# Kernel tuning notes

Hardware: AMD Instinct MI355X
Metric: run time of the kernel (lower is better)

The kernel has to match this reference:

```python
import jax, jax.numpy as jnp
import numpy as np

N = 20000      # n_nodes
L = 4          # lamb_len (number of decay rates)
M = 64         # memory_dimension (= message_dimension)
F = 128        # node feature dim
E = 128        # embedding_dimension
B = 100000     # number of interaction events in the batch
RAW = 2 * M * L + F + 1  # 641, raw message dim
H = RAW // 2   # MLP hidden dim


def setup_inputs() -> dict:
    key = jax.random.key(0)
    ks = jax.random.split(key, 18)
    s = lambda d: 1.0 / np.sqrt(d)
    inp = {
        "node_features": jax.random.normal(ks[0], (N, F), jnp.float32),
        "memory": jax.random.normal(ks[1], (N, L, M), jnp.float32) * 0.1,
        "last_update": jnp.zeros((N,), jnp.float32),
        "lambs": jnp.array([1.0, 0.1, 0.01, 0.001], jnp.float32),
        "theta": jnp.array([0.5], jnp.float32),
        "static_emb": jax.random.normal(ks[2], (N, E), jnp.float32),
        "W1": jax.random.normal(ks[3], (H, RAW), jnp.float32) * s(RAW),
        "b1": jnp.zeros((H,), jnp.float32),
        "W2": jax.random.normal(ks[4], (M, H), jnp.float32) * s(H),
        "b2": jnp.zeros((M,), jnp.float32),
        "We": jax.random.normal(ks[5], (M, L * M), jnp.float32) * s(L * M),
        "be": jnp.zeros((M,), jnp.float32),
        "Ws": jax.random.normal(ks[6], (E, M), jnp.float32) * s(M),
        "bs": jnp.zeros((E,), jnp.float32),
        "timestamps": jax.random.uniform(ks[7], (B,), jnp.float32) * 1000.0,
        "source_nodes": jax.random.randint(ks[8], (B,), 0, N),
        "target_nodes": jax.random.randint(ks[9], (B,), 0, N),
    }
    return inp


def reference(node_features, memory, last_update, lambs, theta, static_emb,
              W1, b1, W2, b2, We, be, Ws, bs,
              timestamps, source_nodes, target_nodes):
    n, l, m = memory.shape
    b = source_nodes.shape[0]
    mem_flat = memory.reshape(n, l * m)

    # ---- temporal memory gather + raw message build: [B, RAW] ----
    src_emb = mem_flat[source_nodes]
    tgt_emb = mem_flat[target_nodes]
    raw = jnp.concatenate(
        [src_emb, tgt_emb, node_features[target_nodes],
         jnp.ones((b, 1), memory.dtype)], axis=1)

    # ---- exp_lambs aggregation per source node ----
    t_node = jax.ops.segment_max(timestamps, source_nodes, num_segments=n)
    counts = jax.ops.segment_sum(jnp.ones_like(timestamps), source_nodes,
                                 num_segments=n)
    has = counts > 0
    t_node_safe = jnp.where(has, t_node, last_update)  # latest event time per node
    dt = t_node_safe[source_nodes] - timestamps        # [B], >= 0
    w = jnp.exp(-dt[:, None] * lambs[None, :])         # [B, L] decay weights
    # decayed sum of raw messages per node, per lambda: [N, L, RAW]
    agg = jnp.stack(
        [jax.ops.segment_sum(w[:, li:li + 1] * raw, source_nodes,
                             num_segments=n) for li in range(l)], axis=1)

    # ---- MLP message function: [N, L, M] ----
    h = jax.nn.relu(jnp.einsum('nlr,hr->nlh', agg, W1) + b1)
    msg = jnp.einsum('nlh,mh->nlm', h, W2) + b2

    # ---- exp memory update ----
    decay = jnp.exp(-(t_node_safe - last_update)[:, None] * lambs[None, :])  # [N, L]
    updated = memory * decay[..., None] + jnp.where(has[:, None, None], msg, 0.0)

    # ---- embedding fusion ----
    dyn = updated.reshape(n, l * m)
    e = jax.nn.leaky_relu(dyn @ We.T + be, negative_slope=0.01)
    s = jax.nn.leaky_relu(e @ Ws.T + bs, negative_slope=0.01)
    embeddings = theta * static_emb + (1.0 - theta) * s
    return embeddings
```

## Files before the change

### kernel.cpp

```cpp
#include <hip/hip_runtime.h>

constexpr int LDIM = 4;
constexpr int MDIM = 64;
constexpr int FDIM = 128;
constexpr int EDIM = 128;
constexpr int RAWD = 641;
constexpr int HDIM = 320;
constexpr int LM   = LDIM * MDIM;
constexpr int KXY  = LM + FDIM;
constexpr int NXY  = 2 * HDIM;

typedef _Float16 f16x8 __attribute__((ext_vector_type(8)));
typedef _Float16 f16x4 __attribute__((ext_vector_type(4)));
typedef float    f32x4 __attribute__((ext_vector_type(4)));

constexpr float WSCALE  = 256.f;
constexpr float WSINV   = 1.f / 256.f;

__global__ void k_init(int* t_node_bits, int* counts, int* cursor2, int* cursor, int Nn)
{
    int n = blockIdx.x * blockDim.x + threadIdx.x;
    if (n < Nn) {
        t_node_bits[n] = 0xBF800000;
        counts[n]  = 0;
        cursor2[n] = 0;
    }
    if (n == 0) cursor[0] = 0;
}

__global__ void k_ev1(const int* __restrict__ src, const float* __restrict__ ts,
                      int* t_node_bits, int* counts, int Bev)
{
    int b = blockIdx.x * blockDim.x + threadIdx.x;
    if (b >= Bev) return;
    int s = src[b];
    atomicMax(&t_node_bits[s], __float_as_int(ts[b]));
    atomicAdd(&counts[s], 1);
}

__global__ void k_node(const int* __restrict__ t_node_bits, const int* __restrict__ counts,
                       const float* __restrict__ last_update, const float* __restrict__ lambs,
                       float* t_safe, float* decay, int* start, int* cursor, int Nn)
{
    int n = blockIdx.x * blockDim.x + threadIdx.x;
    if (n >= Nn) return;
    int c = counts[n];
    float lu = last_update[n];
    float tsn = (c > 0) ? __int_as_float(t_node_bits[n]) : lu;
    t_safe[n] = tsn;
    float d = tsn - lu;
    #pragma unroll
    for (int li = 0; li < LDIM; ++li)
        decay[n * LDIM + li] = expf(-d * lambs[li]);
    start[n] = atomicAdd(cursor, c);
}

__global__ void k_ev2(const int* __restrict__ src, const int* __restrict__ tgt,
                      const float* __restrict__ ts, const float* __restrict__ t_safe,
                      const int* __restrict__ start, int* cursor2,
                      const float* __restrict__ lambs,
                      int* sorted_tgt, float4* sorted_w, int Bev)
{
    int b = blockIdx.x * blockDim.x + threadIdx.x;
    if (b >= Bev) return;
    int s = src[b];
    int pos = start[s] + atomicAdd(&cursor2[s], 1);
    sorted_tgt[pos] = tgt[b];
    float dt = t_safe[s] - ts[b];
    sorted_w[pos] = make_float4(expf(-dt * lambs[0]), expf(-dt * lambs[1]),
                                expf(-dt * lambs[2]), expf(-dt * lambs[3]));
}

__global__ void k_prep(const float* __restrict__ W1, const float* __restrict__ W2,
                       const float* __restrict__ We, const float* __restrict__ Ws,
                       const float* __restrict__ mem, const float* __restrict__ nf,
                       _Float16* WpH, _Float16* WpL, _Float16* W2H, _Float16* W2L,
                       _Float16* WeH, _Float16* WeL, _Float16* WsH, _Float16* WsL,
                       _Float16* A1, int packtot)
{
    int idx = blockIdx.x * blockDim.x + threadIdx.x;
    constexpr int T1 = NXY * KXY;
    constexpr int T2 = MDIM * HDIM;
    constexpr int T3 = MDIM * LM;
    constexpr int T4 = EDIM * MDIM;
    constexpr int TW = T1 + T2 + T3 + T4;
    if (idx < TW) {
        float v; _Float16 *H, *L; int o;
        if (idx < T1) {
            int n = idx / KXY, k = idx % KXY;
            if (n < HDIM) {
                v = (k < LM) ? W1[(long)n * RAWD + k] : 0.f;
            } else {
                int hh = n - HDIM;
                v = (k < LM) ? W1[(long)hh * RAWD + LM + k]
                             : W1[(long)hh * RAWD + 2 * LM + (k - LM)];
            }
            H = WpH; L = WpL; o = idx;
        } else if (idx < T1 + T2) {
            o = idx - T1; v = W2[o]; H = W2H; L = W2L;
        } else if (idx < T1 + T2 + T3) {
            o = idx - T1 - T2; v = We[o]; H = WeH; L = WeL;
        } else {
            o = idx - T1 - T2 - T3; v = Ws[o]; H = WsH; L = WsL;
        }
        float xs = WSCALE * v;
        _Float16 hh = (_Float16)xs;
        _Float16 ll = (_Float16)(xs - (float)hh);
        H[o] = hh; L[o] = ll;
    } else {
        int r = idx - TW;
        if (r < packtot) {
            int n = r / KXY, k = r % KXY;
            float v = (k < LM) ? mem[(long)n * LM + k] : nf[(long)n * FDIM + (k - LM)];
            A1[r] = (_Float16)v;
        }
    }
}

__global__ __launch_bounds__(256) void k_gather(
    const _Float16* __restrict__ C1, const float4* __restrict__ sorted_w,
    const int* __restrict__ sorted_tgt, const int* __restrict__ startb,
    const int* __restrict__ counts,
    const float* __restrict__ W1, const float* __restrict__ b1,
    _Float16* __restrict__ h, int Nn)
{
    const int lane = threadIdx.x & 63;
    const int wv   = threadIdx.x >> 6;
    float4 b4 = *(const float4*)&b1[lane * 4];
    float bbA[4] = {b4.x, b4.y, b4.z, b4.w};
    float bbB = b1[256 + lane];
    float wlA[4], wlB;
    #pragma unroll
    for (int j = 0; j < 4; ++j)
        wlA[j] = W1[(long)(lane * 4 + j) * RAWD + (RAWD - 1)];
    wlB = W1[(long)(256 + lane) * RAWD + (RAWD - 1)];

    for (int n = blockIdx.x * 4 + wv; n < Nn; n += gridDim.x * 4) {
        int cnt = counts[n];
        if (cnt == 0) continue;
        int st = startb[n];
        float zA[4][4], zB[4], sw[4];
        #pragma unroll
        for (int li = 0; li < 4; ++li) { zB[li] = 0.f; sw[li] = 0.f; }
        #pragma unroll
        for (int j = 0; j < 4; ++j)
            #pragma unroll
            for (int li = 0; li < 4; ++li) zA[j][li] = 0.f;

        for (int e = 0; e < cnt; ++e) {
            float4 w = sorted_w[st + e];
            int    t = sorted_tgt[st + e];
            const _Float16* yr = C1 + (long)t * NXY + HDIM;
            f16x4 yA = *(const f16x4*)(yr + lane * 4);
            float  yB = (float)yr[256 + lane];
            float wf[4] = {w.x, w.y, w.z, w.w};
            sw[0] += w.x; sw[1] += w.y; sw[2] += w.z; sw[3] += w.w;
            #pragma unroll
            for (int j = 0; j < 4; ++j) {
                float yv = (float)yA[j];
                #pragma unroll
                for (int li = 0; li < 4; ++li) zA[j][li] += wf[li] * yv;
            }
            #pragma unroll
            for (int li = 0; li < 4; ++li) zB[li] += wf[li] * yB;
        }

        const _Float16* xr = C1 + (long)n * NXY;
        f16x4 xA4 = *(const f16x4*)(xr + lane * 4);
        float xB = (float)xr[256 + lane] + wlB;
        float xA[4];
        #pragma unroll
        for (int j = 0; j < 4; ++j) xA[j] = (float)xA4[j] + wlA[j];
        #pragma unroll
        for (int li = 0; li < 4; ++li) {
            _Float16* hr = h + ((long)n * LDIM + li) * HDIM;
            f16x4 hv;
            #pragma unroll
            for (int j = 0; j < 4; ++j)
                hv[j] = (_Float16)fmaxf(xA[j] * sw[li] + zA[j][li] + bbA[j], 0.f);
            *(f16x4*)(hr + lane * 4) = hv;
            hr[256 + lane] = (_Float16)fmaxf(xB * sw[li] + zB[li] + bbB, 0.f);
        }
    }
}

template <int BM, int BN, int WM, int WN, int EPI>
__global__ __launch_bounds__(256) void k_mgemm(
    const _Float16* __restrict__ Ag,
    const _Float16* __restrict__ Bgh, const _Float16* __restrict__ Bgl,
    _Float16* __restrict__ Ch, float* __restrict__ Cf,
    int M, int N, int K,
    const float* __restrict__ bias, const _Float16* __restrict__ x1h,
    const float* __restrict__ x1f, const float* __restrict__ x2,
    const int* __restrict__ icnts, const float* __restrict__ theta)
{
    constexpr int BK = 32;
    constexpr int WROWS = BM / WM, WCOLS = BN / WN;
    constexpr int SM = WROWS / 16, SN = WCOLS / 16;
    static_assert(WM * WN == 4 && SM * 16 == WROWS && SN * 16 == WCOLS, "");
    static_assert((BM * 4) % 256 == 0 && (BN * 4) % 256 == 0, "");
    __shared__ _Float16 Ash[BM * BK];
    __shared__ _Float16 Bsh[BN * BK], Bsl[BN * BK];
    const int tid  = threadIdx.x;
    const int w    = tid >> 6, lane = tid & 63;
    const int wm   = w / WN,   wn   = w % WN;
    const int lrow = lane & 15, lq = lane >> 4;
    const long m0 = (long)blockIdx.x * BM;
    const int  n0 = blockIdx.y * BN;

    f32x4 acc[SM][SN];
    #pragma unroll
    for (int s = 0; s < SM; ++s)
        #pragma unroll
        for (int t = 0; t < SN; ++t) acc[s][t] = (f32x4){0.f, 0.f, 0.f, 0.f};

    for (int k0 = 0; k0 < K; k0 += BK) {
        #pragma unroll
        for (int f0 = 0; f0 < BM * 4; f0 += 256) {
            int c = f0 + tid;
            int row = c >> 2, kc = c & 3;
            long gm = m0 + row; if (gm > M - 1) gm = M - 1;
            int soff = row * BK + ((kc ^ ((row >> 1) & 3)) << 3);
            *(int4*)&Ash[soff] = *(const int4*)(Ag + gm * (long)K + k0 + kc * 8);
        }
        #pragma unroll
        for (int f0 = 0; f0 < BN * 4; f0 += 256) {
            int c = f0 + tid;
            int row = c >> 2, kc = c & 3;
            long goff = (long)(n0 + row) * K + k0 + kc * 8;
            int soff = row * BK + ((kc ^ ((row >> 1) & 3)) << 3);
            *(int4*)&Bsh[soff] = *(const int4*)(Bgh + goff);
            *(int4*)&Bsl[soff] = *(const int4*)(Bgl + goff);
        }
        __syncthreads();

        f16x8 a[SM], bh[SN], bl[SN];
        #pragma unroll
        for (int s = 0; s < SM; ++s) {
            int row = wm * WROWS + s * 16 + lrow;
            a[s] = *(const f16x8*)&Ash[row * BK + ((lq ^ ((row >> 1) & 3)) << 3)];
        }
        #pragma unroll
        for (int t = 0; t < SN; ++t) {
            int row = wn * WCOLS + t * 16 + lrow;
            int off = row * BK + ((lq ^ ((row >> 1) & 3)) << 3);
            bh[t] = *(const f16x8*)&Bsh[off];
            bl[t] = *(const f16x8*)&Bsl[off];
        }
        #pragma unroll
        for (int s = 0; s < SM; ++s)
            #pragma unroll
            for (int t = 0; t < SN; ++t) {
                acc[s][t] = __builtin_amdgcn_mfma_f32_16x16x32_f16(a[s], bh[t], acc[s][t], 0, 0, 0);
                acc[s][t] = __builtin_amdgcn_mfma_f32_16x16x32_f16(a[s], bl[t], acc[s][t], 0, 0, 0);
            }
        __syncthreads();
    }

    float th = 0.f;
    if constexpr (EPI == 3) th = theta[0];
    #pragma unroll
    for (int s = 0; s < SM; ++s) {
        #pragma unroll
        for (int t = 0; t < SN; ++t) {
            #pragma unroll
            for (int r = 0; r < 4; ++r) {
                long grow = m0 + wm * WROWS + s * 16 + lq * 4 + r;
                if (grow >= M) continue;
                int col = n0 + wn * WCOLS + t * 16 + lrow;
                float v = acc[s][t][r] * WSINV;
                long idx = grow * (long)N + col;
                if constexpr (EPI == 0) {
                    Ch[idx] = (_Float16)v;
                } else if constexpr (EPI == 1) {
                    float vb = v + bias[col];
                    bool has = icnts[grow >> 2] > 0;
                    float mv = (float)x1h[(grow >> 2) * KXY + (grow & 3) * MDIM + col];
                    float u = mv * x2[grow] + (has ? vb : 0.f);
                    Ch[idx] = (_Float16)u;
                } else if constexpr (EPI == 2) {
                    float u = v + bias[col];
                    u = u > 0.f ? u : 0.01f * u;
                    Ch[idx] = (_Float16)u;
                } else {
                    float u = v + bias[col];
                    u = u > 0.f ? u : 0.01f * u;
                    Cf[idx] = th * x1f[idx] + (1.f - th) * u;
                }
            }
        }
    }
}

extern "C" void kernel_launch(void* const* d_in, const int* in_sizes, int n_in,
                              void* d_out, int out_size, void* d_ws, size_t ws_size,
                              hipStream_t stream)
{
    (void)n_in; (void)out_size; (void)ws_size;
    const float* node_features = (const float*)d_in[0];
    const float* memory        = (const float*)d_in[1];
    const float* last_update   = (const float*)d_in[2];
    const float* lambs         = (const float*)d_in[3];
    const float* theta         = (const float*)d_in[4];
    const float* static_emb    = (const float*)d_in[5];
    const float* W1            = (const float*)d_in[6];
    const float* b1            = (const float*)d_in[7];
    const float* W2            = (const float*)d_in[8];
    const float* b2            = (const float*)d_in[9];
    const float* We            = (const float*)d_in[10];
    const float* be            = (const float*)d_in[11];
    const float* Ws            = (const float*)d_in[12];
    const float* bs            = (const float*)d_in[13];
    const float* timestamps    = (const float*)d_in[14];
    const int*   src           = (const int*)d_in[15];
    const int*   tgt           = (const int*)d_in[16];
    float* out = (float*)d_out;

    const int Nn  = in_sizes[2];
    const int Bev = in_sizes[14];

    char* base = (char*)d_ws;
    size_t off = 0;
    auto take = [&](size_t bytes) -> void* {
        off = (off + 255) & ~(size_t)255;
        void* r = base + off;
        off += bytes;
        return r;
    };
    int*    t_node_bits = (int*)   take((size_t)Nn * 4);
    int*    counts      = (int*)   take((size_t)Nn * 4);
    int*    startb      = (int*)   take((size_t)Nn * 4);
    int*    cursor2     = (int*)   take((size_t)Nn * 4);
    int*    cursor      = (int*)   take(256);
    float*  t_safe      = (float*) take((size_t)Nn * 4);
    float*  decay       = (float*) take((size_t)Nn * LDIM * 4);
    int*    sorted_tgt  = (int*)   take((size_t)Bev * 4);
    float4* sorted_w    = (float4*)take((size_t)Bev * 16);
    _Float16* WpH = (_Float16*)take((size_t)NXY * KXY * 2);
    _Float16* WpL = (_Float16*)take((size_t)NXY * KXY * 2);
    _Float16* W2H = (_Float16*)take((size_t)MDIM * HDIM * 2);
    _Float16* W2L = (_Float16*)take((size_t)MDIM * HDIM * 2);
    _Float16* WeH = (_Float16*)take((size_t)MDIM * LM * 2);
    _Float16* WeL = (_Float16*)take((size_t)MDIM * LM * 2);
    _Float16* WsH = (_Float16*)take((size_t)EDIM * MDIM * 2);
    _Float16* WsL = (_Float16*)take((size_t)EDIM * MDIM * 2);
    _Float16* A1  = (_Float16*)take((size_t)Nn * KXY * 2);
    _Float16* C1  = (_Float16*)take((size_t)Nn * NXY * 2);
    _Float16* hbuf= (_Float16*)take((size_t)Nn * LDIM * HDIM * 2);
    _Float16* updh= (_Float16*)take((size_t)Nn * LM * 2);
    _Float16* ebuf= (_Float16*)take((size_t)Nn * MDIM * 2);

    const int tb = 256;
    k_init<<<(Nn + tb - 1) / tb, tb, 0, stream>>>(t_node_bits, counts, cursor2, cursor, Nn);
    k_ev1<<<(Bev + tb - 1) / tb, tb, 0, stream>>>(src, timestamps, t_node_bits, counts, Bev);
    k_node<<<(Nn + tb - 1) / tb, tb, 0, stream>>>(t_node_bits, counts, last_update, lambs,
                                                  t_safe, decay, startb, cursor, Nn);
    k_ev2<<<(Bev + tb - 1) / tb, tb, 0, stream>>>(src, tgt, timestamps, t_safe,
                                                  startb, cursor2, lambs,
                                                  sorted_tgt, sorted_w, Bev);
    const int packtot = Nn * KXY;
    const int preptot = NXY * KXY + MDIM * HDIM + MDIM * LM + EDIM * MDIM + packtot;
    k_prep<<<(preptot + tb - 1) / tb, tb, 0, stream>>>(W1, W2, We, Ws,
                                                       memory, node_features,
                                                       WpH, WpL, W2H, W2L,
                                                       WeH, WeL, WsH, WsL,
                                                       A1, packtot);

    const int mb64 = (Nn + 63) / 64;

    k_mgemm<64, 128, 1, 4, 0><<<dim3(mb64, NXY / 128), 256, 0, stream>>>(
        A1, WpH, WpL, C1, nullptr, Nn, NXY, KXY,
        nullptr, nullptr, nullptr, nullptr, nullptr, nullptr);

    k_gather<<<5000, 256, 0, stream>>>(C1, sorted_w, sorted_tgt, startb, counts,
                                       W1, b1, hbuf, Nn);

    k_mgemm<64, 64, 2, 2, 1><<<dim3(Nn * LDIM / 64, 1), 256, 0, stream>>>(
        hbuf, W2H, W2L, updh, nullptr, Nn * LDIM, MDIM, HDIM,
        b2, A1, nullptr, decay, counts, nullptr);

    k_mgemm<64, 64, 2, 2, 2><<<dim3(mb64, 1), 256, 0, stream>>>(
        updh, WeH, WeL, ebuf, nullptr, Nn, MDIM, LM,
        be, nullptr, nullptr, nullptr, nullptr, nullptr);

    k_mgemm<64, 128, 1, 4, 3><<<dim3(mb64, 1), 256, 0, stream>>>(
        ebuf, WsH, WsL, nullptr, out, Nn, EDIM, MDIM,
        bs, nullptr, static_emb, nullptr, nullptr, theta);
}
```

Measured before the change: 276.2 us.

## Fuse gather/hidden computation with W2 MFMA and memory-update epilogue

Merges the gather kernel that produced the hidden activations with the W2 GEMM. Each block now handles 4 nodes, keeps their 16x320 hidden rows in LDS, and runs the W2 product with MFMA directly before applying decay, bias and the has-event mask. This removes the global hbuf round trip (N*4*320 halves) and one kernel launch. In exchange, W2 hi/lo fragments are read from global memory by every block, and the grid becomes one block per 4 nodes with no grid-stride loop.

Result: slower. 296.0 us (+7.2%).

```diff
diff --git a/kernel.cpp b/kernel.cpp
--- a/kernel.cpp
+++ b/kernel.cpp
@@ -117,15 +117,21 @@
     }
 }
 
-__global__ __launch_bounds__(256) void k_gather(
+__global__ __launch_bounds__(256) void k_gmsg(
     const _Float16* __restrict__ C1, const float4* __restrict__ sorted_w,
     const int* __restrict__ sorted_tgt, const int* __restrict__ startb,
     const int* __restrict__ counts,
     const float* __restrict__ W1, const float* __restrict__ b1,
-    _Float16* __restrict__ h, int Nn)
-{
+    const _Float16* __restrict__ W2H, const _Float16* __restrict__ W2L,
+    const float* __restrict__ b2, const _Float16* __restrict__ A1,
+    const float* __restrict__ decay, _Float16* __restrict__ updh, int Nn)
+{
+    constexpr int HP = HDIM + 8;
+    __shared__ _Float16 hs[16][HP];
     const int lane = threadIdx.x & 63;
     const int wv   = threadIdx.x >> 6;
+    const int n    = blockIdx.x * 4 + wv;
+
     float4 b4 = *(const float4*)&b1[lane * 4];
     float bbA[4] = {b4.x, b4.y, b4.z, b4.w};
     float bbB = b1[256 + lane];
@@ -135,9 +141,14 @@
         wlA[j] = W1[(long)(lane * 4 + j) * RAWD + (RAWD - 1)];
     wlB = W1[(long)(256 + lane) * RAWD + (RAWD - 1)];
 
-    for (int n = blockIdx.x * 4 + wv; n < Nn; n += gridDim.x * 4) {
-        int cnt = counts[n];
-        if (cnt == 0) continue;
+    int cnt = (n < Nn) ? counts[n] : 0;
+    if (cnt == 0) {
+        #pragma unroll
+        for (int li = 0; li < 4; ++li) {
+            *(f16x4*)&hs[wv * 4 + li][lane * 4] = (f16x4){0, 0, 0, 0};
+            hs[wv * 4 + li][256 + lane] = (_Float16)0.f;
+        }
+    } else {
         int st = startb[n];
         float zA[4][4], zB[4], sw[4];
         #pragma unroll
@@ -173,14 +184,40 @@
         for (int j = 0; j < 4; ++j) xA[j] = (float)xA4[j] + wlA[j];
         #pragma unroll
         for (int li = 0; li < 4; ++li) {
-            _Float16* hr = h + ((long)n * LDIM + li) * HDIM;
             f16x4 hv;
             #pragma unroll
             for (int j = 0; j < 4; ++j)
                 hv[j] = (_Float16)fmaxf(xA[j] * sw[li] + zA[j][li] + bbA[j], 0.f);
-            *(f16x4*)(hr + lane * 4) = hv;
-            hr[256 + lane] = (_Float16)fmaxf(xB * sw[li] + zB[li] + bbB, 0.f);
-        }
+            *(f16x4*)&hs[wv * 4 + li][lane * 4] = hv;
+            hs[wv * 4 + li][256 + lane] = (_Float16)fmaxf(xB * sw[li] + zB[li] + bbB, 0.f);
+        }
+    }
+    __syncthreads();
+
+    const int lrow = lane & 15, lq = lane >> 4;
+    f32x4 acc = (f32x4){0.f, 0.f, 0.f, 0.f};
+    for (int k0 = 0; k0 < HDIM; k0 += 32) {
+        f16x8 a = *(const f16x8*)&hs[lrow][k0 + lq * 8];
+        long bo = (long)(wv * 16 + lrow) * HDIM + k0 + lq * 8;
+        f16x8 bh = *(const f16x8*)&W2H[bo];
+        f16x8 bl = *(const f16x8*)&W2L[bo];
+        acc = __builtin_amdgcn_mfma_f32_16x16x32_f16(a, bh, acc, 0, 0, 0);
+        acc = __builtin_amdgcn_mfma_f32_16x16x32_f16(a, bl, acc, 0, 0, 0);
+    }
+
+    int m = wv * 16 + lrow;
+    float bb2 = b2[m];
+    #pragma unroll
+    for (int r = 0; r < 4; ++r) {
+        int r16 = lq * 4 + r;
+        int nib = r16 >> 2, li = r16 & 3;
+        int gn = blockIdx.x * 4 + nib;
+        if (gn >= Nn) continue;
+        float v = acc[r] * WSINV + bb2;
+        bool has = counts[gn] > 0;
+        float mv = (float)A1[(long)gn * KXY + li * MDIM + m];
+        float u = mv * decay[gn * 4 + li] + (has ? v : 0.f);
+        updh[((long)gn * 4 + li) * MDIM + m] = (_Float16)u;
     }
 }
 
@@ -190,9 +227,8 @@
     const _Float16* __restrict__ Bgh, const _Float16* __restrict__ Bgl,
     _Float16* __restrict__ Ch, float* __restrict__ Cf,
     int M, int N, int K,
-    const float* __restrict__ bias, const _Float16* __restrict__ x1h,
-    const float* __restrict__ x1f, const float* __restrict__ x2,
-    const int* __restrict__ icnts, const float* __restrict__ theta)
+    const float* __restrict__ bias, const float* __restrict__ x1f,
+    const float* __restrict__ theta)
 {
     constexpr int BK = 32;
     constexpr int WROWS = BM / WM, WCOLS = BN / WN;
@@ -272,12 +308,6 @@
                 long idx = grow * (long)N + col;
                 if constexpr (EPI == 0) {
                     Ch[idx] = (_Float16)v;
-                } else if constexpr (EPI == 1) {
-                    float vb = v + bias[col];
-                    bool has = icnts[grow >> 2] > 0;
-                    float mv = (float)x1h[(grow >> 2) * KXY + (grow & 3) * MDIM + col];
-                    float u = mv * x2[grow] + (has ? vb : 0.f);
-                    Ch[idx] = (_Float16)u;
                 } else if constexpr (EPI == 2) {
                     float u = v + bias[col];
                     u = u > 0.f ? u : 0.01f * u;
@@ -346,7 +376,6 @@
     _Float16* WsL = (_Float16*)take((size_t)EDIM * MDIM * 2);
     _Float16* A1  = (_Float16*)take((size_t)Nn * KXY * 2);
     _Float16* C1  = (_Float16*)take((size_t)Nn * NXY * 2);
-    _Float16* hbuf= (_Float16*)take((size_t)Nn * LDIM * HDIM * 2);
     _Float16* updh= (_Float16*)take((size_t)Nn * LM * 2);
     _Float16* ebuf= (_Float16*)take((size_t)Nn * MDIM * 2);
 
@@ -370,20 +399,16 @@
 
     k_mgemm<64, 128, 1, 4, 0><<<dim3(mb64, NXY / 128), 256, 0, stream>>>(
         A1, WpH, WpL, C1, nullptr, Nn, NXY, KXY,
-        nullptr, nullptr, nullptr, nullptr, nullptr, nullptr);
-
-    k_gather<<<5000, 256, 0, stream>>>(C1, sorted_w, sorted_tgt, startb, counts,
-                                       W1, b1, hbuf, Nn);
-
-    k_mgemm<64, 64, 2, 2, 1><<<dim3(Nn * LDIM / 64, 1), 256, 0, stream>>>(
-        hbuf, W2H, W2L, updh, nullptr, Nn * LDIM, MDIM, HDIM,
-        b2, A1, nullptr, decay, counts, nullptr);
+        nullptr, nullptr, nullptr);
+
+    k_gmsg<<<(Nn + 3) / 4, 256, 0, stream>>>(C1, sorted_w, sorted_tgt, startb, counts,
+                                             W1, b1, W2H, W2L, b2, A1, decay, updh, Nn);
 
     k_mgemm<64, 64, 2, 2, 2><<<dim3(mb64, 1), 256, 0, stream>>>(
         updh, WeH, WeL, ebuf, nullptr, Nn, MDIM, LM,
-        be, nullptr, nullptr, nullptr, nullptr, nullptr);
+        be, nullptr, nullptr);
 
     k_mgemm<64, 128, 1, 4, 3><<<dim3(mb64, 1), 256, 0, stream>>>(
         ebuf, WsH, WsL, nullptr, out, Nn, EDIM, MDIM,
-        bs, nullptr, static_emb, nullptr, nullptr, theta);
-}
+        bs, static_emb, theta);
+}
```
